# Kernel optimization log

Hardware: AMD Instinct MI355X
Metric: run time of the kernel (lower is better)

## Reference

```python
import jax, jax.numpy as jnp
import numpy as np

NUM_HEADS = 32
NUM_KV_HEADS = 8
HEAD_DIM = 128
HIDDEN = 4096
B, L = 2, 4096


def _phi(x):
    # feature map: elu(x) + 1
    return jax.nn.elu(x) + 1.0


def setup_inputs() -> dict:
    key = jax.random.key(0)
    ks = jax.random.split(key, 9)
    s = 1.0 / np.sqrt(HIDDEN)
    return {
        "hidden_states": jax.random.normal(ks[0], (B, L, HIDDEN), jnp.float32),
        "Wq": jax.random.normal(ks[1], (HIDDEN, HIDDEN), jnp.float32) * s,
        "bq": jnp.zeros((HIDDEN,), jnp.float32),
        "Wk": jax.random.normal(ks[2], (NUM_KV_HEADS * HEAD_DIM, HIDDEN), jnp.float32) * s,
        "bk": jnp.zeros((NUM_KV_HEADS * HEAD_DIM,), jnp.float32),
        "Wv": jax.random.normal(ks[3], (NUM_KV_HEADS * HEAD_DIM, HIDDEN), jnp.float32) * s,
        "bv": jnp.zeros((NUM_KV_HEADS * HEAD_DIM,), jnp.float32),
        "Wo": jax.random.normal(ks[4], (HIDDEN, HIDDEN), jnp.float32) * s,
        "bo": jnp.zeros((HIDDEN,), jnp.float32),
    }


def reference(hidden_states, Wq, bq, Wk, bk, Wv, bv, Wo, bo):
    bsz, q_len, _ = hidden_states.shape
    n_rep = NUM_HEADS // NUM_KV_HEADS

    # projections (nn.Linear: y = x @ W.T + b)
    q = hidden_states @ Wq.T + bq          # [B, L, H*D]
    k = hidden_states @ Wk.T + bk          # [B, L, Hkv*D]
    v = hidden_states @ Wv.T + bv

    q = q.reshape(bsz, q_len, NUM_HEADS, HEAD_DIM).transpose(0, 2, 1, 3)       # [B,H,L,D]
    k = k.reshape(bsz, q_len, NUM_KV_HEADS, HEAD_DIM).transpose(0, 2, 1, 3)    # [B,Hkv,L,D]
    v = v.reshape(bsz, q_len, NUM_KV_HEADS, HEAD_DIM).transpose(0, 2, 1, 3)

    # repeat_kv: [B,Hkv,L,D] -> [B,H,L,D]
    k = jnp.broadcast_to(k[:, :, None], (bsz, NUM_KV_HEADS, n_rep, q_len, HEAD_DIM)).reshape(bsz, NUM_HEADS, q_len, HEAD_DIM)
    v = jnp.broadcast_to(v[:, :, None], (bsz, NUM_KV_HEADS, n_rep, q_len, HEAD_DIM)).reshape(bsz, NUM_HEADS, q_len, HEAD_DIM)

    q = _phi(q)
    k = _phi(k)

    # global KV summary: O(L*d^2) linear attention
    key_value = jnp.einsum('bhld,bhlv->bhvd', k, v)           # [B,H,D,D]
    attn = jnp.einsum('bhqd,bhvd->bhqv', q, key_value)        # [B,H,L,D]

    # normalizer: sum of feature-mapped keys over sequence, per channel
    normalizer = k.sum(axis=2)[:, :, None, :]                  # [B,H,1,D]
    attn = attn / (normalizer + 1e-10)

    attn = attn.transpose(0, 2, 1, 3).reshape(bsz, q_len, HIDDEN)
    return attn @ Wo.T + bo
```

## Files before the change

kernel.cpp:

```cpp
#include <hip/hip_runtime.h>

#define HIDDEN 4096
#define NKV 8
#define NH 32
#define HD 128
#define BATCH 2
#define SEQ 4096
#define ROWS (BATCH*SEQ)

typedef short bf16x8 __attribute__((ext_vector_type(8)));
typedef float f32x4 __attribute__((ext_vector_type(4)));

static __device__ __forceinline__ float bf2f(unsigned short u) {
    union { unsigned int i; float f; } c; c.i = ((unsigned int)u) << 16; return c.f;
}
static __device__ __forceinline__ unsigned short f2bf(float x) {
    union { float f; unsigned int i; } c; c.f = x;
    unsigned int r = c.i + 0x7fffu + ((c.i >> 16) & 1u);
    return (unsigned short)(r >> 16);
}

static __device__ __forceinline__ void gl2lds16(const void* g, void* l) {
    __builtin_amdgcn_global_load_lds(
        (const __attribute__((address_space(1))) unsigned int*)g,
        (__attribute__((address_space(3))) unsigned int*)l, 16, 0, 0);
}

#define WGBAR() __builtin_amdgcn_s_barrier()
#define VMW(n) asm volatile("s_waitcnt vmcnt(" #n ")" ::: "memory")
#define SCHED_FENCE() __builtin_amdgcn_sched_barrier(0)

struct CastSegs {
    const float* in[5];
    unsigned short* out[5];
    int n4[5];
    int cum[5];
    int total;
};

__global__ __launch_bounds__(256)
void cast5_kernel(CastSegs s) {
    int idx = blockIdx.x * blockDim.x + threadIdx.x;
    int stride = gridDim.x * blockDim.x;
    for (int i = idx; i < s.total; i += stride) {
        int seg = 0;
        if (i >= s.cum[1]) seg = 1;
        if (i >= s.cum[2]) seg = 2;
        if (i >= s.cum[3]) seg = 3;
        if (i >= s.cum[4]) seg = 4;
        int j = i - s.cum[seg];
        float4 f = ((const float4*)s.in[seg])[j];
        ushort4 o;
        o.x = f2bf(f.x); o.y = f2bf(f.y); o.z = f2bf(f.z); o.w = f2bf(f.w);
        ((ushort4*)s.out[seg])[j] = o;
    }
}

template<int MODE>
__global__ __launch_bounds__(512, 2)
void gemm256(const unsigned short* __restrict__ A, int lda,
             const unsigned short* __restrict__ B, int ldb,
             const float* __restrict__ bias0, const float* __restrict__ bias1,
             void* __restrict__ Cout, int M, int N, int K)
{
    __shared__ __align__(16) unsigned char sm[131072];

    const int tid = threadIdx.x;
    const int wid = tid >> 6, lane = tid & 63;
    const int wr = wid >> 2, wc = wid & 3;
    const int lr = lane & 15, kg = lane >> 4;
    const int lswz = (lane & 7) << 4;

    int nbx = N >> 8;
    int nwg = nbx * (M >> 8);
    int cpx = nwg >> 3;
    int bid = (int)blockIdx.x;
    int wg = (bid & 7) * cpx + (bid >> 3);
    int bx = wg % nbx, by = wg / nbx;
    int rowBase = by << 8, colBase = bx << 8;

    size_t sA[2][2], sB[2][2];
#pragma unroll
    for (int h = 0; h < 2; ++h)
#pragma unroll
        for (int i = 0; i < 2; ++i) {
            int o = i * 8192 + wid * 1024 + lane * 16;
            int row = o >> 7;
            int ce = ((o & 127) ^ ((row & 7) << 4)) >> 1;
            sA[h][i] = (size_t)(rowBase + h * 128 + row) * lda + ce;
            sB[h][i] = (size_t)(colBase + h * 128 + row) * ldb + ce;
        }
    const int ldsW = wid * 1024;

    auto SA = [&](int nb, int h, int i, size_t ko) {
        gl2lds16(A + sA[h][i] + ko, sm + nb + h * 16384 + i * 8192 + ldsW);
    };
    auto SB = [&](int nb, int h, int i, size_t ko) {
        gl2lds16(B + sB[h][i] + ko, sm + nb + 32768 + h * 16384 + i * 8192 + ldsW);
    };
    auto STAGE = [&](int buf, size_t ko) {
        int nb = buf << 16;
        SB(nb, 0, 0, ko); SB(nb, 0, 1, ko); SB(nb, 1, 0, ko); SB(nb, 1, 1, ko);
        SA(nb, 0, 0, ko); SA(nb, 1, 0, ko); SA(nb, 0, 1, ko); SA(nb, 1, 1, ko);
    };

    const int aRd = wr * 16384 + (lr << 7);
    const int bRd = 32768 + (wc >> 1) * 16384 + (((wc & 1) * 64 + lr) << 7);
    const int kcol0 = (kg * 16) ^ lswz;
    const int kcol1 = (64 + kg * 16) ^ lswz;

    auto RA = [&](int cb, int mp, int ks) -> bf16x8 {
        return *(const bf16x8*)(sm + cb + aRd + mp * 2048 + (ks ? kcol1 : kcol0));
    };
    auto RB = [&](int cb, int n, int ks) -> bf16x8 {
        return *(const bf16x8*)(sm + cb + bRd + n * 2048 + (ks ? kcol1 : kcol0));
    };

    f32x4 acc[8][4] = {};
    bf16x8 bfr[4][2];

    auto MF = [&](bf16x8 a0, bf16x8 a1, bf16x8 a2, bf16x8 a3, int m0, int m1) {
#pragma unroll
        for (int n = 0; n < 4; ++n) {
            acc[m0][n] = __builtin_amdgcn_mfma_f32_16x16x32_bf16(a0, bfr[n][0], acc[m0][n], 0, 0, 0);
            acc[m0][n] = __builtin_amdgcn_mfma_f32_16x16x32_bf16(a1, bfr[n][1], acc[m0][n], 0, 0, 0);
            acc[m1][n] = __builtin_amdgcn_mfma_f32_16x16x32_bf16(a2, bfr[n][0], acc[m1][n], 0, 0, 0);
            acc[m1][n] = __builtin_amdgcn_mfma_f32_16x16x32_bf16(a3, bfr[n][1], acc[m1][n], 0, 0, 0);
        }
    };

    const int NT = K >> 6;

    STAGE(0, 0);
    VMW(0);
    WGBAR();
    SCHED_FENCE();

    int cur = 0;
    for (int t = 0; t < NT; ++t) {
        const int cb = cur << 16;
        if (t + 1 < NT) {
            STAGE(cur ^ 1, (size_t)(t + 1) * 64);
        }
        bf16x8 a0 = RA(cb, 0, 0), a1 = RA(cb, 0, 1), a2 = RA(cb, 1, 0), a3 = RA(cb, 1, 1);
#pragma unroll
        for (int n = 0; n < 4; ++n) { bfr[n][0] = RB(cb, n, 0); bfr[n][1] = RB(cb, n, 1); }
        bf16x8 b0 = RA(cb, 2, 0), b1 = RA(cb, 2, 1), b2 = RA(cb, 3, 0), b3 = RA(cb, 3, 1);
        MF(a0, a1, a2, a3, 0, 1);
        a0 = RA(cb, 4, 0); a1 = RA(cb, 4, 1); a2 = RA(cb, 5, 0); a3 = RA(cb, 5, 1);
        MF(b0, b1, b2, b3, 2, 3);
        b0 = RA(cb, 6, 0); b1 = RA(cb, 6, 1); b2 = RA(cb, 7, 0); b3 = RA(cb, 7, 1);
        MF(a0, a1, a2, a3, 4, 5);
        MF(b0, b1, b2, b3, 6, 7);
        if (t + 1 < NT) {
            VMW(0);
            WGBAR();
            SCHED_FENCE();
        }
        cur ^= 1;
    }

    int r0 = rowBase + wr * 128 + kg * 4;
    int c0 = colBase + wc * 64 + lr;
#pragma unroll
    for (int n = 0; n < 4; ++n) {
        int col = c0 + n * 16;
        float bv;
        if (MODE == 2) bv = (col < 1024) ? bias0[col] : bias1[col - 1024];
        else           bv = bias0[col];
#pragma unroll
        for (int m = 0; m < 8; ++m) {
            int row = r0 + m * 16;
#pragma unroll
            for (int r = 0; r < 4; ++r) {
                float v = acc[m][n][r] + bv;
                if (MODE == 1) v = (v > 0.f) ? v + 1.f : __expf(v);
                if (MODE == 2 && col < 1024) v = (v > 0.f) ? v + 1.f : __expf(v);
                if (MODE == 0) ((float*)Cout)[(size_t)(row + r) * N + col] = v;
                else ((unsigned short*)Cout)[(size_t)(row + r) * N + col] = f2bf(v);
            }
        }
    }
}

__global__ __launch_bounds__(256)
void kv_partial(const unsigned short* __restrict__ Kb, const unsigned short* __restrict__ Vb,
                int ld, float* __restrict__ kvp, float* __restrict__ ksp)
{
    int chunk = blockIdx.x;
    int g = blockIdx.y;
    int b = g >> 3, hkv = g & 7;
    __shared__ float kl[32][128];
    __shared__ float vl[32][128];
    int tid = threadIdx.x;
    int c0 = (tid >> 4) * 8, d0 = (tid & 15) * 8;
    float acc[8][8] = {};
    float ksacc = 0.0f;
    size_t rowBase = (size_t)b * SEQ + (size_t)chunk * 128;

    for (int sch = 0; sch < 4; ++sch) {
        __syncthreads();
        for (int t = tid; t < 512; t += 256) {
            int l = t >> 4, col = (t & 15) * 8;
            size_t off = (rowBase + sch * 32 + l) * ld + hkv * HD + col;
            uint4 kr = *(const uint4*)(Kb + off);
            uint4 vr = *(const uint4*)(Vb + off);
            unsigned int ku[4] = {kr.x, kr.y, kr.z, kr.w};
            unsigned int vu[4] = {vr.x, vr.y, vr.z, vr.w};
#pragma unroll
            for (int q = 0; q < 4; ++q) {
                kl[l][col + q * 2]     = bf2f((unsigned short)(ku[q] & 0xffff));
                kl[l][col + q * 2 + 1] = bf2f((unsigned short)(ku[q] >> 16));
                vl[l][col + q * 2]     = bf2f((unsigned short)(vu[q] & 0xffff));
                vl[l][col + q * 2 + 1] = bf2f((unsigned short)(vu[q] >> 16));
            }
        }
        __syncthreads();
        for (int l = 0; l < 32; ++l) {
            float vv[8], kk[8];
#pragma unroll
            for (int x = 0; x < 8; ++x) { vv[x] = vl[l][c0 + x]; kk[x] = kl[l][d0 + x]; }
#pragma unroll
            for (int x = 0; x < 8; ++x)
#pragma unroll
                for (int y = 0; y < 8; ++y)
                    acc[x][y] += vv[x] * kk[y];
        }
        if (tid < 128) {
            for (int l = 0; l < 32; ++l) ksacc += kl[l][tid];
        }
    }
    float* out = kvp + ((size_t)g * 32 + chunk) * (HD * HD);
#pragma unroll
    for (int x = 0; x < 8; ++x)
#pragma unroll
        for (int y = 0; y < 8; ++y)
            out[(c0 + x) * HD + d0 + y] = acc[x][y];
    if (tid < 128) ksp[((size_t)g * 32 + chunk) * HD + tid] = ksacc;
}

__global__ __launch_bounds__(256)
void kv_reduce(const float* __restrict__ kvp, const float* __restrict__ ksp,
               unsigned short* __restrict__ kvb, float* __restrict__ ksum)
{
    int slice = blockIdx.x;
    int g = blockIdx.y;
    int tid = threadIdx.x;
    int e = slice * 1024 + tid * 4;
    float4 s = {0.f, 0.f, 0.f, 0.f};
    for (int ch = 0; ch < 32; ++ch) {
        float4 p = *(const float4*)(kvp + ((size_t)g * 32 + ch) * (HD * HD) + e);
        s.x += p.x; s.y += p.y; s.z += p.z; s.w += p.w;
    }
    ushort4 o;
    o.x = f2bf(s.x); o.y = f2bf(s.y); o.z = f2bf(s.z); o.w = f2bf(s.w);
    *(ushort4*)(kvb + (size_t)g * HD * HD + e) = o;
    if (slice == 0 && tid < 128) {
        float ss = 0.f;
        for (int ch = 0; ch < 32; ++ch) ss += ksp[((size_t)g * 32 + ch) * HD + tid];
        ksum[g * HD + tid] = ss;
    }
}

__global__ __launch_bounds__(256)
void attn_gemm(const unsigned short* __restrict__ Q,
               const unsigned short* __restrict__ KV,
               const float* __restrict__ KS,
               unsigned short* __restrict__ Out)
{
    const int BK = 32;
    __shared__ unsigned short As[128 * BK];
    __shared__ unsigned short Bs[128 * BK];

    int rt = blockIdx.x;
    int h  = blockIdx.y;
    int g = (rt >> 5) * NKV + (h >> 2);
    int rowBase = rt << 7;

    const unsigned short* A = Q + (size_t)h * HD;
    const unsigned short* B = KV + (size_t)g * HD * HD;
    const float* ks = KS + g * HD;

    int tid = threadIdx.x;
    int wave = tid >> 6, lane = tid & 63;
    int wr = wave >> 1, wc = wave & 1;

    f32x4 acc[4][4] = {};

    int sr = lane >> 2;
    int sc = (lane & 3) * 8;

    const unsigned short* Aw = A + (size_t)(rowBase + wave * 32 + sr) * HIDDEN + sc;
    const unsigned short* Bw = B + (size_t)(wave * 32 + sr) * HD + sc;
    unsigned short* Asw = As + wave * 32 * BK;
    unsigned short* Bsw = Bs + wave * 32 * BK;

    int arow = (wr * 64 + (lane & 15)) * BK + (lane >> 4) * 8;
    int brow = (wc * 64 + (lane & 15)) * BK + (lane >> 4) * 8;

    for (int kt = 0; kt < HD; kt += BK) {
        gl2lds16(Aw + kt, Asw);
        gl2lds16(Aw + kt + (size_t)16 * HIDDEN, Asw + 16 * BK);
        gl2lds16(Bw + kt, Bsw);
        gl2lds16(Bw + kt + (size_t)16 * HD, Bsw + 16 * BK);
        __syncthreads();
        bf16x8 af[4], bfr[4];
#pragma unroll
        for (int i = 0; i < 4; ++i) af[i] = *(const bf16x8*)&As[arow + i * 16 * BK];
#pragma unroll
        for (int j = 0; j < 4; ++j) bfr[j] = *(const bf16x8*)&Bs[brow + j * 16 * BK];
#pragma unroll
        for (int i = 0; i < 4; ++i)
#pragma unroll
            for (int j = 0; j < 4; ++j)
                acc[i][j] = __builtin_amdgcn_mfma_f32_16x16x32_bf16(af[i], bfr[j], acc[i][j], 0, 0, 0);
        __syncthreads();
    }

    int r0 = rowBase + wr * 64 + ((lane >> 4) << 2);
    int c0 = wc * 64 + (lane & 15);
#pragma unroll
    for (int j = 0; j < 4; ++j) {
        int col = c0 + j * 16;
        float inv = 1.0f / (ks[col] + 1e-10f);
#pragma unroll
        for (int i = 0; i < 4; ++i) {
            int row = r0 + i * 16;
#pragma unroll
            for (int r = 0; r < 4; ++r) {
                float v = acc[i][j][r] * inv;
                Out[(size_t)(row + r) * HIDDEN + h * HD + col] = f2bf(v);
            }
        }
    }
}

extern "C" void kernel_launch(void* const* d_in, const int* in_sizes, int n_in,
                              void* d_out, int out_size, void* d_ws, size_t ws_size,
                              hipStream_t stream)
{
    const float* hs = (const float*)d_in[0];
    const float* Wq = (const float*)d_in[1];
    const float* bq = (const float*)d_in[2];
    const float* Wk = (const float*)d_in[3];
    const float* bk = (const float*)d_in[4];
    const float* Wv = (const float*)d_in[5];
    const float* bv = (const float*)d_in[6];
    const float* Wo = (const float*)d_in[7];
    const float* bo = (const float*)d_in[8];

    char* ws = (char*)d_ws;
    size_t off = 0;
    auto alloc = [&](size_t bytes) -> char* {
        char* p = ws + off;
        off += (bytes + 255) & ~(size_t)255;
        return p;
    };

    unsigned short* hs_b  = (unsigned short*)alloc((size_t)ROWS * HIDDEN * 2);
    unsigned short* Wq_b  = (unsigned short*)alloc((size_t)HIDDEN * HIDDEN * 2);
    unsigned short* Wkv_b = (unsigned short*)alloc((size_t)2048 * HIDDEN * 2);
    unsigned short* Wo_b  = (unsigned short*)alloc((size_t)HIDDEN * HIDDEN * 2);
    unsigned short* kvout = (unsigned short*)alloc((size_t)ROWS * 2048 * 2);
    float* ksp   = (float*)alloc((size_t)16 * 32 * HD * 4);
    unsigned short* kvb = (unsigned short*)alloc((size_t)16 * HD * HD * 2);
    float* ksum  = (float*)alloc((size_t)16 * HD * 4);

    float* kvp = (float*)Wq_b;
    unsigned short* attn_b = hs_b;
    unsigned short* q_b = (unsigned short*)d_out;

    (void)in_sizes; (void)n_in; (void)out_size; (void)ws_size;

    CastSegs cs;
    cs.in[0] = hs;  cs.out[0] = hs_b;                         cs.n4[0] = (ROWS * HIDDEN) / 4;
    cs.in[1] = Wq;  cs.out[1] = Wq_b;                         cs.n4[1] = (HIDDEN * HIDDEN) / 4;
    cs.in[2] = Wk;  cs.out[2] = Wkv_b;                        cs.n4[2] = (1024 * HIDDEN) / 4;
    cs.in[3] = Wv;  cs.out[3] = Wkv_b + (size_t)1024 * HIDDEN; cs.n4[3] = (1024 * HIDDEN) / 4;
    cs.in[4] = Wo;  cs.out[4] = Wo_b;                         cs.n4[4] = (HIDDEN * HIDDEN) / 4;
    cs.cum[0] = 0;
    for (int i = 1; i < 5; ++i) cs.cum[i] = cs.cum[i - 1] + cs.n4[i - 1];
    cs.total = cs.cum[4] + cs.n4[4];
    cast5_kernel<<<dim3(2048), dim3(256), 0, stream>>>(cs);

    gemm256<1><<<dim3(512), dim3(512), 0, stream>>>(hs_b, HIDDEN, Wq_b, HIDDEN, bq, nullptr, q_b, ROWS, HIDDEN, HIDDEN);
    gemm256<2><<<dim3(256), dim3(512), 0, stream>>>(hs_b, HIDDEN, Wkv_b, HIDDEN, bk, bv, kvout, ROWS, 2048, HIDDEN);

    kv_partial<<<dim3(32, 16), dim3(256), 0, stream>>>(kvout, kvout + 1024, 2048, kvp, ksp);
    kv_reduce<<<dim3(16, 16), dim3(256), 0, stream>>>(kvp, ksp, kvb, ksum);

    attn_gemm<<<dim3(64, 32), dim3(256), 0, stream>>>(q_b, kvb, ksum, attn_b);

    gemm256<0><<<dim3(512), dim3(512), 0, stream>>>(attn_b, HIDDEN, Wo_b, HIDDEN, bo, nullptr, d_out, ROWS, HIDDEN, HIDDEN);
}
```

Before: 760.1 us.

## Load GEMM B operand directly from global memory into registers instead of LDS

Stops staging the B tile through shared memory. Each wave now reads its B fragments straight from global memory into registers every k-step, which halves the LDS footprint (128KB to 64KB) and removes the B LDS writes and reads. The cost is redundant global/L2 traffic, since the waves sharing a column tile each reload the same B rows, and those global loads are issued without prefetch, so their latency is exposed within the iteration. The smaller LDS use could allow more occupancy, but the launch bounds remain (512,2).

New measurement: 1.194 ms. 57.1% more time.

```diff
diff --git a/kernel.cpp b/kernel.cpp
--- a/kernel.cpp
+++ b/kernel.cpp
@@ -63,7 +63,7 @@
              const float* __restrict__ bias0, const float* __restrict__ bias1,
              void* __restrict__ Cout, int M, int N, int K)
 {
-    __shared__ __align__(16) unsigned char sm[131072];
+    __shared__ __align__(16) unsigned char sm[65536];
 
     const int tid = threadIdx.x;
     const int wid = tid >> 6, lane = tid & 63;
@@ -79,7 +79,7 @@
     int bx = wg % nbx, by = wg / nbx;
     int rowBase = by << 8, colBase = bx << 8;
 
-    size_t sA[2][2], sB[2][2];
+    size_t sA[2][2];
 #pragma unroll
     for (int h = 0; h < 2; ++h)
 #pragma unroll
@@ -88,33 +88,27 @@
             int row = o >> 7;
             int ce = ((o & 127) ^ ((row & 7) << 4)) >> 1;
             sA[h][i] = (size_t)(rowBase + h * 128 + row) * lda + ce;
-            sB[h][i] = (size_t)(colBase + h * 128 + row) * ldb + ce;
         }
     const int ldsW = wid * 1024;
 
-    auto SA = [&](int nb, int h, int i, size_t ko) {
-        gl2lds16(A + sA[h][i] + ko, sm + nb + h * 16384 + i * 8192 + ldsW);
+    auto STAGE = [&](int buf, size_t ko) {
+        int nb = buf << 15;
+        gl2lds16(A + sA[0][0] + ko, sm + nb + 0 * 16384 + 0 * 8192 + ldsW);
+        gl2lds16(A + sA[0][1] + ko, sm + nb + 0 * 16384 + 1 * 8192 + ldsW);
+        gl2lds16(A + sA[1][0] + ko, sm + nb + 1 * 16384 + 0 * 8192 + ldsW);
+        gl2lds16(A + sA[1][1] + ko, sm + nb + 1 * 16384 + 1 * 8192 + ldsW);
     };
-    auto SB = [&](int nb, int h, int i, size_t ko) {
-        gl2lds16(B + sB[h][i] + ko, sm + nb + 32768 + h * 16384 + i * 8192 + ldsW);
-    };
-    auto STAGE = [&](int buf, size_t ko) {
-        int nb = buf << 16;
-        SB(nb, 0, 0, ko); SB(nb, 0, 1, ko); SB(nb, 1, 0, ko); SB(nb, 1, 1, ko);
-        SA(nb, 0, 0, ko); SA(nb, 1, 0, ko); SA(nb, 0, 1, ko); SA(nb, 1, 1, ko);
-    };
 
     const int aRd = wr * 16384 + (lr << 7);
-    const int bRd = 32768 + (wc >> 1) * 16384 + (((wc & 1) * 64 + lr) << 7);
     const int kcol0 = (kg * 16) ^ lswz;
     const int kcol1 = (64 + kg * 16) ^ lswz;
 
     auto RA = [&](int cb, int mp, int ks) -> bf16x8 {
         return *(const bf16x8*)(sm + cb + aRd + mp * 2048 + (ks ? kcol1 : kcol0));
     };
-    auto RB = [&](int cb, int n, int ks) -> bf16x8 {
-        return *(const bf16x8*)(sm + cb + bRd + n * 2048 + (ks ? kcol1 : kcol0));
-    };
+
+    const unsigned short* Bw = B + (size_t)(colBase + wc * 64 + lr) * ldb + kg * 8;
+    const size_t bstep = (size_t)16 * ldb;
 
     f32x4 acc[8][4] = {};
     bf16x8 bfr[4][2];
@@ -138,13 +132,18 @@
 
     int cur = 0;
     for (int t = 0; t < NT; ++t) {
-        const int cb = cur << 16;
+        const int cb = cur << 15;
+        const size_t kt = (size_t)t * 64;
         if (t + 1 < NT) {
-            STAGE(cur ^ 1, (size_t)(t + 1) * 64);
+            STAGE(cur ^ 1, kt + 64);
+        }
+        const unsigned short* Bt = Bw + kt;
+#pragma unroll
+        for (int n = 0; n < 4; ++n) {
+            bfr[n][0] = *(const bf16x8*)(Bt + (size_t)n * bstep);
+            bfr[n][1] = *(const bf16x8*)(Bt + (size_t)n * bstep + 32);
         }
         bf16x8 a0 = RA(cb, 0, 0), a1 = RA(cb, 0, 1), a2 = RA(cb, 1, 0), a3 = RA(cb, 1, 1);
-#pragma unroll
-        for (int n = 0; n < 4; ++n) { bfr[n][0] = RB(cb, n, 0); bfr[n][1] = RB(cb, n, 1); }
         bf16x8 b0 = RA(cb, 2, 0), b1 = RA(cb, 2, 1), b2 = RA(cb, 3, 0), b3 = RA(cb, 3, 1);
         MF(a0, a1, a2, a3, 0, 1);
         a0 = RA(cb, 4, 0); a1 = RA(cb, 4, 1); a2 = RA(cb, 5, 0); a3 = RA(cb, 5, 1);
```

## Fuse Q and KV projection GEMMs into one launch; swizzle attn_gemm LDS

Applied to the files above, without the earlier changes.

Merges the separate Q and K/V projection GEMMs into a single 768-workgroup launch with N=6144. The epilogue routes columns to the Q buffer or the KV buffer and applies the elu+1 feature map only to Q and K columns. This removes one launch and the tail imbalance of two separate grids. It assumes the bf16 Wq and Wkv weights sit contiguously in the workspace. It also XOR-swizzles the LDS layout in attn_gemm to cut bank conflicts on fragment reads.

New measurement: 774.0 us. About the same (+1.8%).

```diff
diff --git a/kernel.cpp b/kernel.cpp
--- a/kernel.cpp
+++ b/kernel.cpp
@@ -61,7 +61,9 @@
 void gemm256(const unsigned short* __restrict__ A, int lda,
              const unsigned short* __restrict__ B, int ldb,
              const float* __restrict__ bias0, const float* __restrict__ bias1,
-             void* __restrict__ Cout, int M, int N, int K)
+             const float* __restrict__ bias2,
+             void* __restrict__ Cout, void* __restrict__ Cout2,
+             int M, int N, int K)
 {
     __shared__ __align__(16) unsigned char sm[131072];
 
@@ -166,7 +168,8 @@
     for (int n = 0; n < 4; ++n) {
         int col = c0 + n * 16;
         float bv;
-        if (MODE == 2) bv = (col < 1024) ? bias0[col] : bias1[col - 1024];
+        if (MODE == 3) bv = (col < 4096) ? bias0[col]
+                          : (col < 5120) ? bias1[col - 4096] : bias2[col - 5120];
         else           bv = bias0[col];
 #pragma unroll
         for (int m = 0; m < 8; ++m) {
@@ -174,10 +177,15 @@
 #pragma unroll
             for (int r = 0; r < 4; ++r) {
                 float v = acc[m][n][r] + bv;
-                if (MODE == 1) v = (v > 0.f) ? v + 1.f : __expf(v);
-                if (MODE == 2 && col < 1024) v = (v > 0.f) ? v + 1.f : __expf(v);
-                if (MODE == 0) ((float*)Cout)[(size_t)(row + r) * N + col] = v;
-                else ((unsigned short*)Cout)[(size_t)(row + r) * N + col] = f2bf(v);
+                if (MODE == 3) {
+                    if (col < 5120) v = (v > 0.f) ? v + 1.f : __expf(v);
+                    if (col < 4096)
+                        ((unsigned short*)Cout)[(size_t)(row + r) * 4096 + col] = f2bf(v);
+                    else
+                        ((unsigned short*)Cout2)[(size_t)(row + r) * 2048 + (col - 4096)] = f2bf(v);
+                } else {
+                    ((float*)Cout)[(size_t)(row + r) * N + col] = v;
+                }
             }
         }
     }
@@ -288,15 +296,16 @@
     f32x4 acc[4][4] = {};
 
     int sr = lane >> 2;
-    int sc = (lane & 3) * 8;
+    int sc = ((lane & 3) ^ ((lane >> 3) & 3)) * 8;
 
     const unsigned short* Aw = A + (size_t)(rowBase + wave * 32 + sr) * HIDDEN + sc;
     const unsigned short* Bw = B + (size_t)(wave * 32 + sr) * HD + sc;
     unsigned short* Asw = As + wave * 32 * BK;
     unsigned short* Bsw = Bs + wave * 32 * BK;
 
-    int arow = (wr * 64 + (lane & 15)) * BK + (lane >> 4) * 8;
-    int brow = (wc * 64 + (lane & 15)) * BK + (lane >> 4) * 8;
+    const int kgs = ((lane >> 4) ^ (((lane & 15) >> 1) & 3)) * 8;
+    int arow = (wr * 64 + (lane & 15)) * BK + kgs;
+    int brow = (wc * 64 + (lane & 15)) * BK + kgs;
 
     for (int kt = 0; kt < HD; kt += BK) {
         gl2lds16(Aw + kt, Asw);
@@ -383,13 +392,16 @@
     cs.total = cs.cum[4] + cs.n4[4];
     cast5_kernel<<<dim3(2048), dim3(256), 0, stream>>>(cs);
 
-    gemm256<1><<<dim3(512), dim3(512), 0, stream>>>(hs_b, HIDDEN, Wq_b, HIDDEN, bq, nullptr, q_b, ROWS, HIDDEN, HIDDEN);
-    gemm256<2><<<dim3(256), dim3(512), 0, stream>>>(hs_b, HIDDEN, Wkv_b, HIDDEN, bk, bv, kvout, ROWS, 2048, HIDDEN);
+    gemm256<3><<<dim3(768), dim3(512), 0, stream>>>(hs_b, HIDDEN, Wq_b, HIDDEN,
+                                                    bq, bk, bv, q_b, kvout,
+                                                    ROWS, 6144, HIDDEN);
 
     kv_partial<<<dim3(32, 16), dim3(256), 0, stream>>>(kvout, kvout + 1024, 2048, kvp, ksp);
     kv_reduce<<<dim3(16, 16), dim3(256), 0, stream>>>(kvp, ksp, kvb, ksum);
 
     attn_gemm<<<dim3(64, 32), dim3(256), 0, stream>>>(q_b, kvb, ksum, attn_b);
 
-    gemm256<0><<<dim3(512), dim3(512), 0, stream>>>(attn_b, HIDDEN, Wo_b, HIDDEN, bo, nullptr, d_out, ROWS, HIDDEN, HIDDEN);
-}
+    gemm256<0><<<dim3(512), dim3(512), 0, stream>>>(attn_b, HIDDEN, Wo_b, HIDDEN,
+                                                    bo, nullptr, nullptr, d_out, nullptr,
+                                                    ROWS, HIDDEN, HIDDEN);
+}
```
